# Performance work log

Hardware: AMD Instinct MI355X
Metric: run time of the kernel (lower is better)

## Reference

```python
import jax, jax.numpy as jnp
import numpy as np

B, T, IN, H, OUT = 128, 1024, 17, 512, 17


def setup_inputs() -> dict:
    key = jax.random.key(0)
    ks = jax.random.split(key, 11)
    s_in = 1.0 / np.sqrt(H)
    return {
        "x": jax.random.normal(ks[0], (B, T, IN), dtype=jnp.float32),
        "wih0": jax.random.normal(ks[1], (4 * H, IN), dtype=jnp.float32) * s_in,
        "whh0": jax.random.normal(ks[2], (4 * H, H), dtype=jnp.float32) * s_in,
        "bih0": jax.random.normal(ks[3], (4 * H,), dtype=jnp.float32) * s_in,
        "bhh0": jax.random.normal(ks[4], (4 * H,), dtype=jnp.float32) * s_in,
        "wih1": jax.random.normal(ks[5], (4 * H, H), dtype=jnp.float32) * s_in,
        "whh1": jax.random.normal(ks[6], (4 * H, H), dtype=jnp.float32) * s_in,
        "bih1": jax.random.normal(ks[7], (4 * H,), dtype=jnp.float32) * s_in,
        "bhh1": jax.random.normal(ks[8], (4 * H,), dtype=jnp.float32) * s_in,
        "lin_w": jax.random.normal(ks[9], (OUT, H), dtype=jnp.float32) * s_in,
        "lin_b": jax.random.normal(ks[10], (OUT,), dtype=jnp.float32) * s_in,
    }


def _lstm_layer(x, wih, whh, bih, bhh):
    # x: [B, T, D]; gate order i, f, g, o (torch.nn.LSTMCell convention)
    b, _, _ = x.shape
    h = whh.shape[1]
    # Precompute input projection for all timesteps: [B, T, 4H]
    proj = jnp.einsum("btd,gd->btg", x, wih) + bih

    def step(carry, p_t):
        h_t, c_t = carry
        gates = p_t + h_t @ whh.T + bhh  # [B, 4H]
        i, f, g, o = jnp.split(gates, 4, axis=1)
        i = jax.nn.sigmoid(i)
        f = jax.nn.sigmoid(f)
        o = jax.nn.sigmoid(o)
        g = jnp.tanh(g)
        c_t = f * c_t + i * g
        h_t = o * jnp.tanh(c_t)
        return (h_t, c_t), h_t

    h0 = jnp.zeros((b, h), x.dtype)
    c0 = jnp.zeros((b, h), x.dtype)
    _, ys = jax.lax.scan(step, (h0, c0), jnp.swapaxes(proj, 0, 1))  # ys: [T, B, H]
    return jnp.swapaxes(ys, 0, 1)  # [B, T, H]


def reference(x, wih0, whh0, bih0, bhh0, wih1, whh1, bih1, bhh1, lin_w, lin_b):
    y = _lstm_layer(x, wih0, whh0, bih0, bhh0)
    y = _lstm_layer(y, wih1, whh1, bih1, bhh1)
    h_last = y[:, -1, :]  # [B, H]
    return h_last @ lin_w.T + lin_b  # [B, OUT]
```

## Files before the change

kernel.cpp:

```cpp
#include <hip/hip_runtime.h>
#include <cstddef>
#include <cstdint>

typedef unsigned long long ull;
typedef unsigned short u16;
typedef __attribute__((ext_vector_type(8))) short s8v;
typedef __attribute__((ext_vector_type(4))) float f4v;

#define GROUPS 8
#define BG     16
#define JS     16
#define TPB    256
#define NT     1024
#define HDIM   512
#define INDIM  17
#define OUTDIM 17
#define BTOT   128

#define AT_LD(p)   __hip_atomic_load((p), __ATOMIC_RELAXED, __HIP_MEMORY_SCOPE_AGENT)
#define AT_ST(p,v) __hip_atomic_store((p), (v), __ATOMIC_RELAXED, __HIP_MEMORY_SCOPE_AGENT)

#define TILE_U16 8192
#define WIDX(k, b) ((((k) >> 5) * 512) + ((((k) >> 3) & 3) * 128) + ((b) * 8) + ((k) & 7))
#define SLICE(wg)  (((wg) >> 1) * 512 + ((wg) & 1) * 256)

#define FA_OFF     ((size_t)0)
#define FB_OFF     ((size_t)1024)
#define RA_OFF     ((size_t)4096)
#define RING_BYTES ((size_t)4 * GROUPS * 2 * TILE_U16 * 2)
#define RB_OFF     (RA_OFF + RING_BYTES)
#define WS_NEEDED  (RB_OFF + RING_BYTES)
#define RIX(sl, gr, pl) ((((size_t)(sl) * GROUPS + (gr)) * 2 + (pl)) * TILE_U16)

#define L_H0   0
#define L_H1   98304
#define L_EXA  131072
#define L_EXB  135168
#define L_HOA  139264
#define L_HOB  140288
#define L_CTL  141312
#define LDS_SZ 141376

__device__ __forceinline__ u16 f2bf(float f) {
  unsigned int u = __float_as_uint(f);
  u += 0x7FFFu + ((u >> 16) & 1u);
  return (u16)(u >> 16);
}
__device__ __forceinline__ float bf2f(u16 h) {
  return __uint_as_float(((unsigned int)h) << 16);
}
__device__ __forceinline__ float sigm(float x) { return 1.f / (1.f + __expf(-x)); }
__device__ __forceinline__ float tanh_f(float x) { return 2.f / (1.f + __expf(-2.f * x)) - 1.f; }

#define MFMA(a, b, c) __builtin_amdgcn_mfma_f32_16x16x32_bf16((a), (b), (c), 0, 0, 0)

__device__ __forceinline__ void pbar(int* c, int& nbar, int lane) {
  ++nbar;
  if (lane == 0)
    (void)__hip_atomic_fetch_add(c, 1, __ATOMIC_RELEASE, __HIP_MEMORY_SCOPE_WORKGROUP);
  while (__hip_atomic_load(c, __ATOMIC_ACQUIRE, __HIP_MEMORY_SCOPE_WORKGROUP) < 2 * nbar) {}
}

__global__ __launch_bounds__(TPB, 1) void lstm_fused(
    const float* __restrict__ x,
    const float* __restrict__ wih0, const float* __restrict__ whh0,
    const float* __restrict__ bih0, const float* __restrict__ bhh0,
    const float* __restrict__ wih1, const float* __restrict__ whh1,
    const float* __restrict__ bih1, const float* __restrict__ bhh1,
    u16* __restrict__ ringA, u16* __restrict__ ringB,
    int* __restrict__ flagsA, int* __restrict__ flagsB)
{
  const int bid  = blockIdx.x;
  const int gr   = bid & 7;
  const int wg   = bid >> 3;
  const int j0   = wg * JS;
  const int tid  = threadIdx.x;
  const int wave = tid >> 6;
  const int lane = tid & 63;
  const int n    = lane & 15;
  const int q    = lane >> 4;
  const int k0   = q * 8;

  __shared__ __align__(16) char smem[LDS_SZ];
  int* ctl = (int*)(smem + L_CTL);
  float* exgA = (float*)(smem + L_EXA);
  float* exgB = (float*)(smem + L_EXB);

  if (tid < 8) ctl[tid] = 0;

  {
    int b_l = tid >> 4, j_l = tid & 15, jg = j0 + j_l;
    int wo = WIDX(jg, b_l);
    AT_ST(&ringA[RIX(0, gr, 0) + wo], (u16)0);
    AT_ST(&ringA[RIX(0, gr, 1) + wo], (u16)0);
    AT_ST(&ringB[RIX(0, gr, 0) + wo], (u16)0);
    AT_ST(&ringB[RIX(0, gr, 1) + wo], (u16)0);
  }
  __syncthreads();
  if (wave == 0 && lane == 0) AT_ST(flagsA + gr * 32 + wg, 1);
  if (wave == 2 && lane == 0) AT_ST(flagsB + gr * 32 + wg, 1);

  const f4v z = {0.f, 0.f, 0.f, 0.f};
  const int p  = (wave & 1) * 64 + lane;
  const int jq = p & 15, b0 = p >> 4;
  const int jg = j0 + jq;
  const int ho0 = (jq >> 3) * 128 + b0 * 8 + (jq & 7);
  const int ho1 = (jq >> 3) * 128 + (b0 + 8) * 8 + (jq & 7);
  const int slice = SLICE(wg);

  if (wave < 2) {
    const int g0 = wave * 2;
    s8v wx_h[2], wx_l[2];
#pragma unroll
    for (int i = 0; i < 2; ++i) {
      const float* wr = wih0 + (size_t)((g0 + i) * HDIM + j0 + n) * INDIM;
#pragma unroll
      for (int j = 0; j < 8; ++j) {
        int k = k0 + j;
        float v = (k < INDIM) ? wr[k] : 0.f;
        u16 hi = f2bf(v);
        wx_h[i][j] = (short)hi;
        wx_l[i][j] = (short)f2bf(v - bf2f(hi));
      }
    }
    s8v wh_h[2][16], wh_l[2][16];
#pragma unroll
    for (int i = 0; i < 2; ++i) {
      const float* wr = whh0 + (size_t)((g0 + i) * HDIM + j0 + n) * HDIM;
#pragma unroll
      for (int kt = 0; kt < 16; ++kt)
#pragma unroll
        for (int j = 0; j < 8; ++j) {
          float v = wr[kt * 32 + k0 + j];
          u16 hi = f2bf(v);
          wh_h[i][kt][j] = (short)hi;
          wh_l[i][kt][j] = (short)f2bf(v - bf2f(hi));
        }
    }
    float bias[4];
#pragma unroll
    for (int g = 0; g < 4; ++g) bias[g] = bih0[g * HDIM + jg] + bhh0[g * HDIM + jg];
    float c0a = 0.f, c0b = 0.f;
    int nbar = 0;

    for (int s = 1; s <= NT + 1; ++s) {
      f4v xa[2] = {z, z};
      if (s <= NT) {
        const float* xr = x + ((size_t)(gr * BG + n) * NT + (s - 1)) * INDIM;
        s8v axh, axl;
#pragma unroll
        for (int j = 0; j < 8; ++j) {
          int k = k0 + j;
          float v = (k < INDIM) ? xr[k] : 0.f;
          u16 hi = f2bf(v);
          axh[j] = (short)hi;
          axl[j] = (short)f2bf(v - bf2f(hi));
        }
#pragma unroll
        for (int i = 0; i < 2; ++i) {
          xa[i] = MFMA(axh, wx_h[i], xa[i]);
          xa[i] = MFMA(axl, wx_h[i], xa[i]);
          xa[i] = MFMA(axh, wx_l[i], xa[i]);
        }
      }
      if (wave == 0) {
        const int idx = lane & 31;
        const int* pp = (lane < 32) ? (flagsA + gr * 32 + idx)
                                    : (flagsB + gr * 32 + idx);
        const int tgt = (lane < 32) ? s : s - 3;
        while (__ballot(AT_LD(pp) >= tgt) != ~0ULL) __builtin_amdgcn_s_sleep(1);
        __hip_atomic_store(&ctl[2], s, __ATOMIC_RELEASE, __HIP_MEMORY_SCOPE_WORKGROUP);
      } else {
        while (__hip_atomic_load(&ctl[2], __ATOMIC_ACQUIRE, __HIP_MEMORY_SCOPE_WORKGROUP) < s) {}
      }
      const int sl3 = (s - 1) % 3;
      {
        const ull* src = (const ull*)(ringA + RIX((s - 1) & 3, gr, wave));
        char* dst = smem + L_H0 + (sl3 * 2 + wave) * 16384;
#pragma unroll
        for (int r = 0; r < 32; r += 16) {
          ull v[16];
#pragma unroll
          for (int i = 0; i < 16; ++i) v[i] = AT_LD(src + (r + i) * 64 + lane);
#pragma unroll
          for (int i = 0; i < 16; ++i) *(ull*)(dst + ((r + i) * 64 + lane) * 8) = v[i];
        }
      }
      pbar(&ctl[0], nbar, lane);
      if (wave == 0 && lane == 0)
        __hip_atomic_store(&ctl[4 + sl3], s - 1, __ATOMIC_RELEASE,
                           __HIP_MEMORY_SCOPE_WORKGROUP);
      if (s == NT + 1) break;

      const char* sh = smem + L_H0 + (sl3 * 2 + 0) * 16384;
      const char* sl = smem + L_H0 + (sl3 * 2 + 1) * 16384;
      f4v cHH[2] = {z, z}, cLH[2] = {z, z}, cHL[2] = {z, z};
#pragma unroll
      for (int kt = 0; kt < 16; ++kt) {
        s8v ah = *(const s8v*)(sh + kt * 1024 + q * 256 + n * 16);
        s8v al = *(const s8v*)(sl + kt * 1024 + q * 256 + n * 16);
#pragma unroll
        for (int i = 0; i < 2; ++i) {
          cHH[i] = MFMA(ah, wh_h[i][kt], cHH[i]);
          cLH[i] = MFMA(al, wh_h[i][kt], cLH[i]);
          cHL[i] = MFMA(ah, wh_l[i][kt], cHL[i]);
        }
      }
#pragma unroll
      for (int i = 0; i < 2; ++i) {
        f4v e = xa[i] + cHH[i] + cLH[i] + cHL[i];
#pragma unroll
        for (int r = 0; r < 4; ++r)
          exgA[(g0 + i) * 256 + (q * 4 + r) * 16 + n] = e[r];
      }
      pbar(&ctl[0], nbar, lane);
      u16* hoh = (u16*)(smem + L_HOA);
      u16* hol = (u16*)(smem + L_HOA + 512);
      {
        float pi = exgA[0 * 256 + b0 * 16 + jq] + bias[0];
        float pf = exgA[1 * 256 + b0 * 16 + jq] + bias[1];
        float pg = exgA[2 * 256 + b0 * 16 + jq] + bias[2];
        float po = exgA[3 * 256 + b0 * 16 + jq] + bias[3];
        float ig = sigm(pi), fg = sigm(pf), gg = tanh_f(pg), og = sigm(po);
        c0a = fg * c0a + ig * gg;
        float h = og * tanh_f(c0a);
        u16 hh = f2bf(h), hl = f2bf(h - bf2f(hh));
        hoh[ho0] = hh; hol[ho0] = hl;
      }
      {
        float pi = exgA[0 * 256 + (b0 + 8) * 16 + jq] + bias[0];
        float pf = exgA[1 * 256 + (b0 + 8) * 16 + jq] + bias[1];
        float pg = exgA[2 * 256 + (b0 + 8) * 16 + jq] + bias[2];
        float po = exgA[3 * 256 + (b0 + 8) * 16 + jq] + bias[3];
        float ig = sigm(pi), fg = sigm(pf), gg = tanh_f(pg), og = sigm(po);
        c0b = fg * c0b + ig * gg;
        float h = og * tanh_f(c0b);
        u16 hh = f2bf(h), hl = f2bf(h - bf2f(hh));
        hoh[ho1] = hh; hol[ho1] = hl;
      }
      pbar(&ctl[0], nbar, lane);
      if (wave == 0) {
        ull v0 = *(const ull*)(smem + L_HOA + lane * 8);
        ull v1 = *(const ull*)(smem + L_HOA + 512 + lane * 8);
        ull* d0 = (ull*)ringA + ((RIX(s & 3, gr, 0) + slice) >> 2);
        ull* d1 = (ull*)ringA + ((RIX(s & 3, gr, 1) + slice) >> 2);
        AT_ST(d0 + lane, v0);
        AT_ST(d1 + lane, v1);
        __asm__ volatile("s_waitcnt vmcnt(0)" ::: "memory");
        if (lane == 0) AT_ST(flagsA + gr * 32 + wg, s + 1);
      }
    }
  } else {
    const int wv = wave - 2;
    const int g0 = wv * 2;
    s8v w1x[2][16], w1h[2][16];
#pragma unroll
    for (int i = 0; i < 2; ++i) {
      const float* p1 = wih1 + (size_t)((g0 + i) * HDIM + j0 + n) * HDIM;
      const float* p2 = whh1 + (size_t)((g0 + i) * HDIM + j0 + n) * HDIM;
#pragma unroll
      for (int kt = 0; kt < 16; ++kt)
#pragma unroll
        for (int j = 0; j < 8; ++j) {
          w1x[i][kt][j] = (short)f2bf(p1[kt * 32 + k0 + j]);
          w1h[i][kt][j] = (short)f2bf(p2[kt * 32 + k0 + j]);
        }
    }
    float bias[4];
#pragma unroll
    for (int g = 0; g < 4; ++g) bias[g] = bih1[g * HDIM + jg] + bhh1[g * HDIM + jg];
    float c1a = 0.f, c1b = 0.f;
    int nbar = 0;

    for (int t = 1; t <= NT; ++t) {
      if (wave == 2) {
        const int* pp = flagsB + gr * 32 + (lane & 31);
        while (__ballot(AT_LD(pp) >= t) != ~0ULL) __builtin_amdgcn_s_sleep(1);
        __hip_atomic_store(&ctl[3], t, __ATOMIC_RELEASE, __HIP_MEMORY_SCOPE_WORKGROUP);
      } else {
        while (__hip_atomic_load(&ctl[3], __ATOMIC_ACQUIRE, __HIP_MEMORY_SCOPE_WORKGROUP) < t) {}
      }
      {
        const ull* src = (const ull*)(ringB + RIX((t - 1) & 3, gr, wv));
        char* dst = smem + L_H1 + wv * 16384;
#pragma unroll
        for (int r = 0; r < 32; r += 16) {
          ull v[16];
#pragma unroll
          for (int i = 0; i < 16; ++i) v[i] = AT_LD(src + (r + i) * 64 + lane);
#pragma unroll
          for (int i = 0; i < 16; ++i) *(ull*)(dst + ((r + i) * 64 + lane) * 8) = v[i];
        }
      }
      pbar(&ctl[1], nbar, lane);
      const char* th = smem + L_H1;
      const char* tl = smem + L_H1 + 16384;
      f4v dHH[2] = {z, z}, dLH[2] = {z, z};
#pragma unroll
      for (int kt = 0; kt < 16; ++kt) {
        s8v ah = *(const s8v*)(th + kt * 1024 + q * 256 + n * 16);
        s8v al = *(const s8v*)(tl + kt * 1024 + q * 256 + n * 16);
#pragma unroll
        for (int i = 0; i < 2; ++i) {
          dHH[i] = MFMA(ah, w1h[i][kt], dHH[i]);
          dLH[i] = MFMA(al, w1h[i][kt], dLH[i]);
        }
      }
      const int sl3 = t % 3;
      while (__hip_atomic_load(&ctl[4 + sl3], __ATOMIC_ACQUIRE,
                               __HIP_MEMORY_SCOPE_WORKGROUP) < t) {}
      const char* sh = smem + L_H0 + (sl3 * 2 + 0) * 16384;
      const char* sl = smem + L_H0 + (sl3 * 2 + 1) * 16384;
      f4v eHH[2] = {z, z}, eLH[2] = {z, z};
#pragma unroll
      for (int kt = 0; kt < 16; ++kt) {
        s8v ah = *(const s8v*)(sh + kt * 1024 + q * 256 + n * 16);
        s8v al = *(const s8v*)(sl + kt * 1024 + q * 256 + n * 16);
#pragma unroll
        for (int i = 0; i < 2; ++i) {
          eHH[i] = MFMA(ah, w1x[i][kt], eHH[i]);
          eLH[i] = MFMA(al, w1x[i][kt], eLH[i]);
        }
      }
#pragma unroll
      for (int i = 0; i < 2; ++i) {
        f4v e = dHH[i] + dLH[i] + eHH[i] + eLH[i];
#pragma unroll
        for (int r = 0; r < 4; ++r)
          exgB[(g0 + i) * 256 + (q * 4 + r) * 16 + n] = e[r];
      }
      pbar(&ctl[1], nbar, lane);
      u16* hoh = (u16*)(smem + L_HOB);
      u16* hol = (u16*)(smem + L_HOB + 512);
      {
        float pi = exgB[0 * 256 + b0 * 16 + jq] + bias[0];
        float pf = exgB[1 * 256 + b0 * 16 + jq] + bias[1];
        float pg = exgB[2 * 256 + b0 * 16 + jq] + bias[2];
        float po = exgB[3 * 256 + b0 * 16 + jq] + bias[3];
        float ig = sigm(pi), fg = sigm(pf), gg = tanh_f(pg), og = sigm(po);
        c1a = fg * c1a + ig * gg;
        float h = og * tanh_f(c1a);
        u16 hh = f2bf(h), hl = f2bf(h - bf2f(hh));
        hoh[ho0] = hh; hol[ho0] = hl;
      }
      {
        float pi = exgB[0 * 256 + (b0 + 8) * 16 + jq] + bias[0];
        float pf = exgB[1 * 256 + (b0 + 8) * 16 + jq] + bias[1];
        float pg = exgB[2 * 256 + (b0 + 8) * 16 + jq] + bias[2];
        float po = exgB[3 * 256 + (b0 + 8) * 16 + jq] + bias[3];
        float ig = sigm(pi), fg = sigm(pf), gg = tanh_f(pg), og = sigm(po);
        c1b = fg * c1b + ig * gg;
        float h = og * tanh_f(c1b);
        u16 hh = f2bf(h), hl = f2bf(h - bf2f(hh));
        hoh[ho1] = hh; hol[ho1] = hl;
      }
      pbar(&ctl[1], nbar, lane);
      if (wave == 2) {
        ull v0 = *(const ull*)(smem + L_HOB + lane * 8);
        ull v1 = *(const ull*)(smem + L_HOB + 512 + lane * 8);
        ull* d0 = (ull*)ringB + ((RIX(t & 3, gr, 0) + slice) >> 2);
        ull* d1 = (ull*)ringB + ((RIX(t & 3, gr, 1) + slice) >> 2);
        AT_ST(d0 + lane, v0);
        AT_ST(d1 + lane, v1);
        __asm__ volatile("s_waitcnt vmcnt(0)" ::: "memory");
        if (lane == 0) AT_ST(flagsB + gr * 32 + wg, t + 1);
      }
    }
  }
}

__global__ void final_linear(const u16* __restrict__ ringB,
                             const float* __restrict__ lin_w,
                             const float* __restrict__ lin_b,
                             float* __restrict__ out) {
  int b = blockIdx.x, o = threadIdx.x;
  int gr = b >> 4, b_l = b & 15;
  if (o < OUTDIM) {
    float acc = lin_b[o];
    const u16* ph = ringB + RIX(NT & 3, gr, 0);
    const u16* pl = ringB + RIX(NT & 3, gr, 1);
    for (int j = 0; j < HDIM; ++j) {
      int idx = WIDX(j, b_l);
      float h = bf2f(ph[idx]) + bf2f(pl[idx]);
      acc += h * lin_w[(size_t)o * HDIM + j];
    }
    out[b * OUTDIM + o] = acc;
  }
}

__global__ void init_flags(int* __restrict__ f) {
  int i = blockIdx.x * TPB + threadIdx.x;
  if (i < 512) f[i] = 0;
}

__global__ void sentinel_kernel(float* __restrict__ out, int nv) {
  int i = blockIdx.x * TPB + threadIdx.x;
  if (i < nv) out[i] = 1e30f;
}

extern "C" void kernel_launch(void* const* d_in, const int* in_sizes, int n_in,
                              void* d_out, int out_size, void* d_ws, size_t ws_size,
                              hipStream_t stream) {
  (void)in_sizes; (void)n_in;
  const float* x     = (const float*)d_in[0];
  const float* wih0  = (const float*)d_in[1];
  const float* whh0  = (const float*)d_in[2];
  const float* bih0  = (const float*)d_in[3];
  const float* bhh0  = (const float*)d_in[4];
  const float* wih1  = (const float*)d_in[5];
  const float* whh1  = (const float*)d_in[6];
  const float* bih1  = (const float*)d_in[7];
  const float* bhh1  = (const float*)d_in[8];
  const float* lin_w = (const float*)d_in[9];
  const float* lin_b = (const float*)d_in[10];
  float* out = (float*)d_out;
  char* ws = (char*)d_ws;

  if (ws_size < WS_NEEDED) {
    sentinel_kernel<<<(out_size + TPB - 1) / TPB, TPB, 0, stream>>>(out, out_size);
    return;
  }

  int* flagsA = (int*)(ws + FA_OFF);
  int* flagsB = (int*)(ws + FB_OFF);
  u16* ringA  = (u16*)(ws + RA_OFF);
  u16* ringB  = (u16*)(ws + RB_OFF);

  init_flags<<<2, TPB, 0, stream>>>(flagsA);
  lstm_fused<<<256, TPB, 0, stream>>>(x, wih0, whh0, bih0, bhh0,
                                      wih1, whh1, bih1, bhh1,
                                      ringA, ringB, flagsA, flagsB);
  final_linear<<<BTOT, 64, 0, stream>>>(ringB, lin_w, lin_b, out);
}
```

Before: 5.274 ms.

## Drop low-half bf16 split of hidden state and decentralize flag waits

The hidden state was exchanged between workgroups as a bf16 hi/lo pair. It now travels as a single bf16 value, which halves ring traffic, LDS copies and the activation-side MFMAs in both layers. The flag polling is also spread across both waves instead of one leader wave plus an LDS broadcast. Layer 0 now gates on a local layer-1 progress counter instead of polling global layer-1 flags. The final hidden state is written in fp32 to a separate buffer for the linear head, at the cost of lower precision in the recurrent state.

```diff
diff --git a/kernel.cpp b/kernel.cpp
--- a/kernel.cpp
+++ b/kernel.cpp
@@ -27,19 +27,20 @@
 #define FA_OFF     ((size_t)0)
 #define FB_OFF     ((size_t)1024)
 #define RA_OFF     ((size_t)4096)
-#define RING_BYTES ((size_t)4 * GROUPS * 2 * TILE_U16 * 2)
+#define RING_BYTES ((size_t)4 * GROUPS * TILE_U16 * 2)
 #define RB_OFF     (RA_OFF + RING_BYTES)
-#define WS_NEEDED  (RB_OFF + RING_BYTES)
-#define RIX(sl, gr, pl) ((((size_t)(sl) * GROUPS + (gr)) * 2 + (pl)) * TILE_U16)
+#define FB32_OFF   (RB_OFF + RING_BYTES)
+#define WS_NEEDED  (FB32_OFF + (size_t)BTOT * HDIM * 4)
+#define RIX1(sl, gr) (((size_t)(sl) * GROUPS + (gr)) * TILE_U16)
 
 #define L_H0   0
-#define L_H1   98304
-#define L_EXA  131072
-#define L_EXB  135168
-#define L_HOA  139264
-#define L_HOB  140288
-#define L_CTL  141312
-#define LDS_SZ 141376
+#define L_H1   49152
+#define L_EXA  65536
+#define L_EXB  69632
+#define L_HOA  73728
+#define L_HOB  74240
+#define L_CTL  74752
+#define LDS_SZ 74816
 
 __device__ __forceinline__ u16 f2bf(float f) {
   unsigned int u = __float_as_uint(f);
@@ -68,6 +69,7 @@
     const float* __restrict__ wih1, const float* __restrict__ whh1,
     const float* __restrict__ bih1, const float* __restrict__ bhh1,
     u16* __restrict__ ringA, u16* __restrict__ ringB,
+    float* __restrict__ fb32,
     int* __restrict__ flagsA, int* __restrict__ flagsB)
 {
   const int bid  = blockIdx.x;
@@ -91,10 +93,8 @@
   {
     int b_l = tid >> 4, j_l = tid & 15, jg = j0 + j_l;
     int wo = WIDX(jg, b_l);
-    AT_ST(&ringA[RIX(0, gr, 0) + wo], (u16)0);
-    AT_ST(&ringA[RIX(0, gr, 1) + wo], (u16)0);
-    AT_ST(&ringB[RIX(0, gr, 0) + wo], (u16)0);
-    AT_ST(&ringB[RIX(0, gr, 1) + wo], (u16)0);
+    AT_ST(&ringA[RIX1(0, gr) + wo], (u16)0);
+    AT_ST(&ringB[RIX1(0, gr) + wo], (u16)0);
   }
   __syncthreads();
   if (wave == 0 && lane == 0) AT_ST(flagsA + gr * 32 + wg, 1);
@@ -107,6 +107,7 @@
   const int ho0 = (jq >> 3) * 128 + b0 * 8 + (jq & 7);
   const int ho1 = (jq >> 3) * 128 + (b0 + 8) * 8 + (jq & 7);
   const int slice = SLICE(wg);
+  const int half = wave & 1;
 
   if (wave < 2) {
     const int g0 = wave * 2;
@@ -163,28 +164,25 @@
           xa[i] = MFMA(axh, wx_l[i], xa[i]);
         }
       }
-      if (wave == 0) {
-        const int idx = lane & 31;
-        const int* pp = (lane < 32) ? (flagsA + gr * 32 + idx)
-                                    : (flagsB + gr * 32 + idx);
-        const int tgt = (lane < 32) ? s : s - 3;
-        while (__ballot(AT_LD(pp) >= tgt) != ~0ULL) __builtin_amdgcn_s_sleep(1);
-        __hip_atomic_store(&ctl[2], s, __ATOMIC_RELEASE, __HIP_MEMORY_SCOPE_WORKGROUP);
-      } else {
-        while (__hip_atomic_load(&ctl[2], __ATOMIC_ACQUIRE, __HIP_MEMORY_SCOPE_WORKGROUP) < s) {}
+      {
+        const int* pp = flagsA + gr * 32 + half * 16 + (lane & 15);
+        for (;;) {
+          bool ok = AT_LD(pp) >= s;
+          int l1t = __hip_atomic_load(&ctl[7], __ATOMIC_ACQUIRE,
+                                      __HIP_MEMORY_SCOPE_WORKGROUP);
+          if (__ballot(ok) == ~0ULL && l1t >= s - 4) break;
+          __builtin_amdgcn_s_sleep(1);
+        }
       }
       const int sl3 = (s - 1) % 3;
       {
-        const ull* src = (const ull*)(ringA + RIX((s - 1) & 3, gr, wave));
-        char* dst = smem + L_H0 + (sl3 * 2 + wave) * 16384;
-#pragma unroll
-        for (int r = 0; r < 32; r += 16) {
-          ull v[16];
-#pragma unroll
-          for (int i = 0; i < 16; ++i) v[i] = AT_LD(src + (r + i) * 64 + lane);
-#pragma unroll
-          for (int i = 0; i < 16; ++i) *(ull*)(dst + ((r + i) * 64 + lane) * 8) = v[i];
-        }
+        const ull* src = (const ull*)(ringA + RIX1((s - 1) & 3, gr)) + half * 1024;
+        char* dst = smem + L_H0 + sl3 * 16384 + half * 8192;
+        ull v[16];
+#pragma unroll
+        for (int i = 0; i < 16; ++i) v[i] = AT_LD(src + i * 64 + lane);
+#pragma unroll
+        for (int i = 0; i < 16; ++i) *(ull*)(dst + (i * 64 + lane) * 8) = v[i];
       }
       pbar(&ctl[0], nbar, lane);
       if (wave == 0 && lane == 0)
@@ -192,30 +190,26 @@
                            __HIP_MEMORY_SCOPE_WORKGROUP);
       if (s == NT + 1) break;
 
-      const char* sh = smem + L_H0 + (sl3 * 2 + 0) * 16384;
-      const char* sl = smem + L_H0 + (sl3 * 2 + 1) * 16384;
-      f4v cHH[2] = {z, z}, cLH[2] = {z, z}, cHL[2] = {z, z};
+      const char* sh = smem + L_H0 + sl3 * 16384;
+      f4v cHH[2] = {z, z}, cHL[2] = {z, z};
 #pragma unroll
       for (int kt = 0; kt < 16; ++kt) {
         s8v ah = *(const s8v*)(sh + kt * 1024 + q * 256 + n * 16);
-        s8v al = *(const s8v*)(sl + kt * 1024 + q * 256 + n * 16);
 #pragma unroll
         for (int i = 0; i < 2; ++i) {
           cHH[i] = MFMA(ah, wh_h[i][kt], cHH[i]);
-          cLH[i] = MFMA(al, wh_h[i][kt], cLH[i]);
           cHL[i] = MFMA(ah, wh_l[i][kt], cHL[i]);
         }
       }
 #pragma unroll
       for (int i = 0; i < 2; ++i) {
-        f4v e = xa[i] + cHH[i] + cLH[i] + cHL[i];
+        f4v e = xa[i] + cHH[i] + cHL[i];
 #pragma unroll
         for (int r = 0; r < 4; ++r)
           exgA[(g0 + i) * 256 + (q * 4 + r) * 16 + n] = e[r];
       }
       pbar(&ctl[0], nbar, lane);
-      u16* hoh = (u16*)(smem + L_HOA);
-      u16* hol = (u16*)(smem + L_HOA + 512);
+      u16* ho = (u16*)(smem + L_HOA);
       {
         float pi = exgA[0 * 256 + b0 * 16 + jq] + bias[0];
         float pf = exgA[1 * 256 + b0 * 16 + jq] + bias[1];
@@ -223,9 +217,7 @@
         float po = exgA[3 * 256 + b0 * 16 + jq] + bias[3];
         float ig = sigm(pi), fg = sigm(pf), gg = tanh_f(pg), og = sigm(po);
         c0a = fg * c0a + ig * gg;
-        float h = og * tanh_f(c0a);
-        u16 hh = f2bf(h), hl = f2bf(h - bf2f(hh));
-        hoh[ho0] = hh; hol[ho0] = hl;
+        ho[ho0] = f2bf(og * tanh_f(c0a));
       }
       {
         float pi = exgA[0 * 256 + (b0 + 8) * 16 + jq] + bias[0];
@@ -234,25 +226,19 @@
         float po = exgA[3 * 256 + (b0 + 8) * 16 + jq] + bias[3];
         float ig = sigm(pi), fg = sigm(pf), gg = tanh_f(pg), og = sigm(po);
         c0b = fg * c0b + ig * gg;
-        float h = og * tanh_f(c0b);
-        u16 hh = f2bf(h), hl = f2bf(h - bf2f(hh));
-        hoh[ho1] = hh; hol[ho1] = hl;
+        ho[ho1] = f2bf(og * tanh_f(c0b));
       }
       pbar(&ctl[0], nbar, lane);
       if (wave == 0) {
         ull v0 = *(const ull*)(smem + L_HOA + lane * 8);
-        ull v1 = *(const ull*)(smem + L_HOA + 512 + lane * 8);
-        ull* d0 = (ull*)ringA + ((RIX(s & 3, gr, 0) + slice) >> 2);
-        ull* d1 = (ull*)ringA + ((RIX(s & 3, gr, 1) + slice) >> 2);
+        ull* d0 = (ull*)ringA + ((RIX1(s & 3, gr) + slice) >> 2);
         AT_ST(d0 + lane, v0);
-        AT_ST(d1 + lane, v1);
         __asm__ volatile("s_waitcnt vmcnt(0)" ::: "memory");
         if (lane == 0) AT_ST(flagsA + gr * 32 + wg, s + 1);
       }
     }
   } else {
-    const int wv = wave - 2;
-    const int g0 = wv * 2;
+    const int g0 = (wave - 2) * 2;
     s8v w1x[2][16], w1h[2][16];
 #pragma unroll
     for (int i = 0; i < 2; ++i) {
@@ -273,65 +259,48 @@
     int nbar = 0;
 
     for (int t = 1; t <= NT; ++t) {
-      if (wave == 2) {
-        const int* pp = flagsB + gr * 32 + (lane & 31);
+      {
+        const int* pp = flagsB + gr * 32 + half * 16 + (lane & 15);
         while (__ballot(AT_LD(pp) >= t) != ~0ULL) __builtin_amdgcn_s_sleep(1);
-        __hip_atomic_store(&ctl[3], t, __ATOMIC_RELEASE, __HIP_MEMORY_SCOPE_WORKGROUP);
-      } else {
-        while (__hip_atomic_load(&ctl[3], __ATOMIC_ACQUIRE, __HIP_MEMORY_SCOPE_WORKGROUP) < t) {}
-      }
-      {
-        const ull* src = (const ull*)(ringB + RIX((t - 1) & 3, gr, wv));
-        char* dst = smem + L_H1 + wv * 16384;
-#pragma unroll
-        for (int r = 0; r < 32; r += 16) {
-          ull v[16];
-#pragma unroll
-          for (int i = 0; i < 16; ++i) v[i] = AT_LD(src + (r + i) * 64 + lane);
-#pragma unroll
-          for (int i = 0; i < 16; ++i) *(ull*)(dst + ((r + i) * 64 + lane) * 8) = v[i];
-        }
+      }
+      {
+        const ull* src = (const ull*)(ringB + RIX1((t - 1) & 3, gr)) + half * 1024;
+        char* dst = smem + L_H1 + half * 8192;
+        ull v[16];
+#pragma unroll
+        for (int i = 0; i < 16; ++i) v[i] = AT_LD(src + i * 64 + lane);
+#pragma unroll
+        for (int i = 0; i < 16; ++i) *(ull*)(dst + (i * 64 + lane) * 8) = v[i];
       }
       pbar(&ctl[1], nbar, lane);
       const char* th = smem + L_H1;
-      const char* tl = smem + L_H1 + 16384;
-      f4v dHH[2] = {z, z}, dLH[2] = {z, z};
+      f4v dHH[2] = {z, z};
 #pragma unroll
       for (int kt = 0; kt < 16; ++kt) {
         s8v ah = *(const s8v*)(th + kt * 1024 + q * 256 + n * 16);
-        s8v al = *(const s8v*)(tl + kt * 1024 + q * 256 + n * 16);
-#pragma unroll
-        for (int i = 0; i < 2; ++i) {
-          dHH[i] = MFMA(ah, w1h[i][kt], dHH[i]);
-          dLH[i] = MFMA(al, w1h[i][kt], dLH[i]);
-        }
+#pragma unroll
+        for (int i = 0; i < 2; ++i) dHH[i] = MFMA(ah, w1h[i][kt], dHH[i]);
       }
       const int sl3 = t % 3;
       while (__hip_atomic_load(&ctl[4 + sl3], __ATOMIC_ACQUIRE,
                                __HIP_MEMORY_SCOPE_WORKGROUP) < t) {}
-      const char* sh = smem + L_H0 + (sl3 * 2 + 0) * 16384;
-      const char* sl = smem + L_H0 + (sl3 * 2 + 1) * 16384;
-      f4v eHH[2] = {z, z}, eLH[2] = {z, z};
+      const char* sh = smem + L_H0 + sl3 * 16384;
+      f4v eHH[2] = {z, z};
 #pragma unroll
       for (int kt = 0; kt < 16; ++kt) {
         s8v ah = *(const s8v*)(sh + kt * 1024 + q * 256 + n * 16);
-        s8v al = *(const s8v*)(sl + kt * 1024 + q * 256 + n * 16);
-#pragma unroll
-        for (int i = 0; i < 2; ++i) {
-          eHH[i] = MFMA(ah, w1x[i][kt], eHH[i]);
-          eLH[i] = MFMA(al, w1x[i][kt], eLH[i]);
-        }
+#pragma unroll
+        for (int i = 0; i < 2; ++i) eHH[i] = MFMA(ah, w1x[i][kt], eHH[i]);
       }
 #pragma unroll
       for (int i = 0; i < 2; ++i) {
-        f4v e = dHH[i] + dLH[i] + eHH[i] + eLH[i];
+        f4v e = dHH[i] + eHH[i];
 #pragma unroll
         for (int r = 0; r < 4; ++r)
           exgB[(g0 + i) * 256 + (q * 4 + r) * 16 + n] = e[r];
       }
       pbar(&ctl[1], nbar, lane);
-      u16* hoh = (u16*)(smem + L_HOB);
-      u16* hol = (u16*)(smem + L_HOB + 512);
+      u16* ho = (u16*)(smem + L_HOB);
       {
         float pi = exgB[0 * 256 + b0 * 16 + jq] + bias[0];
         float pf = exgB[1 * 256 + b0 * 16 + jq] + bias[1];
@@ -340,8 +309,10 @@
         float ig = sigm(pi), fg = sigm(pf), gg = tanh_f(pg), og = sigm(po);
         c1a = fg * c1a + ig * gg;
         float h = og * tanh_f(c1a);
-        u16 hh = f2bf(h), hl = f2bf(h - bf2f(hh));
-        hoh[ho0] = hh; hol[ho0] = hl;
+        ho[ho0] = f2bf(h);
+        if (t == NT)
+          AT_ST((unsigned int*)&fb32[(size_t)(gr * BG + b0) * HDIM + jg],
+                __float_as_uint(h));
       }
       {
         float pi = exgB[0 * 256 + (b0 + 8) * 16 + jq] + bias[0];
@@ -351,39 +322,36 @@
         float ig = sigm(pi), fg = sigm(pf), gg = tanh_f(pg), og = sigm(po);
         c1b = fg * c1b + ig * gg;
         float h = og * tanh_f(c1b);
-        u16 hh = f2bf(h), hl = f2bf(h - bf2f(hh));
-        hoh[ho1] = hh; hol[ho1] = hl;
+        ho[ho1] = f2bf(h);
+        if (t == NT)
+          AT_ST((unsigned int*)&fb32[(size_t)(gr * BG + b0 + 8) * HDIM + jg],
+                __float_as_uint(h));
       }
       pbar(&ctl[1], nbar, lane);
       if (wave == 2) {
         ull v0 = *(const ull*)(smem + L_HOB + lane * 8);
-        ull v1 = *(const ull*)(smem + L_HOB + 512 + lane * 8);
-        ull* d0 = (ull*)ringB + ((RIX(t & 3, gr, 0) + slice) >> 2);
-        ull* d1 = (ull*)ringB + ((RIX(t & 3, gr, 1) + slice) >> 2);
+        ull* d0 = (ull*)ringB + ((RIX1(t & 3, gr) + slice) >> 2);
         AT_ST(d0 + lane, v0);
-        AT_ST(d1 + lane, v1);
         __asm__ volatile("s_waitcnt vmcnt(0)" ::: "memory");
-        if (lane == 0) AT_ST(flagsB + gr * 32 + wg, t + 1);
+        if (lane == 0) {
+          AT_ST(flagsB + gr * 32 + wg, t + 1);
+          __hip_atomic_store(&ctl[7], t, __ATOMIC_RELEASE,
+                             __HIP_MEMORY_SCOPE_WORKGROUP);
+        }
       }
     }
   }
 }
 
-__global__ void final_linear(const u16* __restrict__ ringB,
+__global__ void final_linear(const float* __restrict__ fb32,
                              const float* __restrict__ lin_w,
                              const float* __restrict__ lin_b,
                              float* __restrict__ out) {
   int b = blockIdx.x, o = threadIdx.x;
-  int gr = b >> 4, b_l = b & 15;
   if (o < OUTDIM) {
     float acc = lin_b[o];
-    const u16* ph = ringB + RIX(NT & 3, gr, 0);
-    const u16* pl = ringB + RIX(NT & 3, gr, 1);
-    for (int j = 0; j < HDIM; ++j) {
-      int idx = WIDX(j, b_l);
-      float h = bf2f(ph[idx]) + bf2f(pl[idx]);
-      acc += h * lin_w[(size_t)o * HDIM + j];
-    }
+    const float* hr = fb32 + (size_t)b * HDIM;
+    for (int j = 0; j < HDIM; ++j) acc += hr[j] * lin_w[(size_t)o * HDIM + j];
     out[b * OUTDIM + o] = acc;
   }
 }
@@ -425,10 +393,11 @@
   int* flagsB = (int*)(ws + FB_OFF);
   u16* ringA  = (u16*)(ws + RA_OFF);
   u16* ringB  = (u16*)(ws + RB_OFF);
+  float* fb32 = (float*)(ws + FB32_OFF);
 
   init_flags<<<2, TPB, 0, stream>>>(flagsA);
   lstm_fused<<<256, TPB, 0, stream>>>(x, wih0, whh0, bih0, bhh0,
                                       wih1, whh1, bih1, bhh1,
-                                      ringA, ringB, flagsA, flagsB);
-  final_linear<<<BTOT, 64, 0, stream>>>(ringB, lin_w, lin_b, out);
-}
+                                      ringA, ringB, fb32, flagsA, flagsB);
+  final_linear<<<BTOT, 64, 0, stream>>>(fb32, lin_w, lin_b, out);
+}
```

New measurement: 6.119 ms. 16.0% more time.
